# Kernel optimization log

Measured on AMD Instinct MI355X. Metric: run time of the kernel, lower is better.

## Reference

```python
import jax, jax.numpy as jnp
import numpy as np

L, D, H, FF, E, K, S, B = 2, 1024, 16, 4096, 8, 2, 1024, 8
HD = D // H
EPS = 1e-5


def setup_inputs() -> dict:
    key = jax.random.key(0)
    ks = jax.random.split(key, 18)
    sc = 0.02
    inp = {
        "src": jax.random.normal(ks[0], (S, B, D), jnp.float32),
        "pos": jax.random.normal(ks[1], (S, B, D), jnp.float32),
        "qkv_w": jax.random.normal(ks[2], (L, 3 * D, D), jnp.float32) * sc,
        "qkv_b": jnp.zeros((L, 3 * D), jnp.float32),
        "out_w": jax.random.normal(ks[3], (L, D, D), jnp.float32) * sc,
        "out_b": jnp.zeros((L, D), jnp.float32),
        "ln1_w": jnp.ones((L, D), jnp.float32),
        "ln1_b": jnp.zeros((L, D), jnp.float32),
        "ln2_w": jnp.ones((L, D), jnp.float32),
        "ln2_b": jnp.zeros((L, D), jnp.float32),
        "gate_w": jax.random.normal(ks[4], (L, E, D), jnp.float32) * sc,
        "gate_b": jnp.zeros((L, E), jnp.float32),
        "w1": jax.random.normal(ks[5], (L, E, FF, D), jnp.float32) * sc,
        "b1": jnp.zeros((L, E, FF), jnp.float32),
        "w2": jax.random.normal(ks[6], (L, E, D, FF), jnp.float32) * sc,
        "b2": jnp.zeros((L, E, D), jnp.float32),
    }
    return inp


def _ln(x, w, b):
    m = x.mean(-1, keepdims=True)
    v = ((x - m) ** 2).mean(-1, keepdims=True)
    return (x - m) * jax.lax.rsqrt(v + EPS) * w + b


def _attn(src, pos, qkv_w, qkv_b, out_w, out_b):
    qk_in = src + pos  # q = k = with_pos_embed(src, pos); v = src
    wq, wk, wv = qkv_w[:D], qkv_w[D:2 * D], qkv_w[2 * D:]
    bq, bk, bv = qkv_b[:D], qkv_b[D:2 * D], qkv_b[2 * D:]
    q = (qk_in @ wq.T + bq).reshape(S, B, H, HD)
    k = (qk_in @ wk.T + bk).reshape(S, B, H, HD)
    v = (src @ wv.T + bv).reshape(S, B, H, HD)
    scores = jnp.einsum("sbhd,tbhd->bhst", q, k) / jnp.sqrt(jnp.float32(HD))
    a = jax.nn.softmax(scores, axis=-1)
    o = jnp.einsum("bhst,tbhd->sbhd", a, v).reshape(S, B, D)
    return o @ out_w.T + out_b


def _moe(x, gate_w, gate_b, w1, b1, w2, b2):
    T = S * B
    xf = x.reshape(T, D)
    scores = xf @ gate_w.T + gate_b                      # [T, E]
    topv, topi = jax.lax.top_k(scores, K)                # [T, K]
    probs = jax.nn.softmax(topv, axis=-1)                # [T, K]
    # combine weight per (token, expert); experts not in top-k get 0
    cw = jnp.zeros((T, E), xf.dtype).at[jnp.arange(T)[:, None], topi].add(probs)
    out = jnp.zeros_like(xf)
    for e in range(E):  # small fixed loop over experts (structurally distinct GEMMs)
        h = jax.nn.relu(xf @ w1[e].T + b1[e])
        y = h @ w2[e].T + b2[e]
        out = out + cw[:, e:e + 1] * y
    return out.reshape(S, B, D), probs, topi


def _aux(probs, topi):
    usage = jnp.zeros(E, probs.dtype).at[topi.reshape(-1)].add(probs.reshape(-1))
    p = usage / usage.sum()
    return -(p * jnp.log(p + 1e-9)).sum()


def reference(src, pos, qkv_w, qkv_b, out_w, out_b, ln1_w, ln1_b, ln2_w, ln2_b,
              gate_w, gate_b, w1, b1, w2, b2):
    x = src
    aux = jnp.float32(0.0)
    for l in range(L):
        a = _attn(x, pos, qkv_w[l], qkv_b[l], out_w[l], out_b[l])
        x = _ln(x + a, ln1_w[l], ln1_b[l])
        m, probs, topi = _moe(x, gate_w[l], gate_b[l], w1[l], b1[l], w2[l], b2[l])
        aux = aux + (1.0 / L) * _aux(probs, topi)
        x = _ln(x + m, ln2_w[l], ln2_b[l])
    return x, aux
```

## Files before the change

### kernel.cpp

```cpp
#include <hip/hip_runtime.h>

#define L_ 2
#define D_ 1024
#define H_ 16
#define FF_ 4096
#define E_ 8
#define S_ 1024
#define B_ 8
#define T_ (S_*B_)
#define TP_ 17408
#define NBLK_MAX 136
#define HALF_BLK 68

typedef _Float16 half8 __attribute__((ext_vector_type(8)));
typedef _Float16 half4_t __attribute__((ext_vector_type(4)));
typedef float f32x4 __attribute__((ext_vector_type(4)));

__device__ __forceinline__ f32x4 mfma16(half8 a, half8 b, f32x4 c) {
  return __builtin_amdgcn_mfma_f32_16x16x32_f16(a, b, c, 0, 0, 0);
}

struct hl2 { _Float16 h, l; };
__device__ __forceinline__ hl2 split2(float v) {
  hl2 r;
  r.h = (_Float16)v;
  r.l = (_Float16)(v - (float)r.h);
  return r;
}

__device__ __forceinline__ void gll16(const _Float16* g, _Float16* l) {
  __builtin_amdgcn_global_load_lds(
      (const __attribute__((address_space(1))) unsigned int*)g,
      (__attribute__((address_space(3))) unsigned int*)l, 16, 0, 0);
}

template<int NPROD, bool GATHER, bool MOE, bool RELU, int OUT>
__global__ __launch_bounds__(256, 4)
void gemm_pl(const _Float16* __restrict__ Ah, const _Float16* __restrict__ Al,
             const float* __restrict__ B, const float* __restrict__ bias,
             float* __restrict__ C, _Float16* __restrict__ Ch,
             _Float16* __restrict__ Cl,
             int K, int N, long bExpStride, int biasExpStride,
             const int* __restrict__ gtok,
             const int* __restrict__ nblk,
             const unsigned char* __restrict__ blk_e, int mb0)
{
  const int mb = blockIdx.x, nb = blockIdx.y;
  const float* Bp = B;
  const float* biasp = bias;
  if constexpr (MOE) {
    if (mb0 + mb >= *nblk) return;
    const int e = blk_e[mb0 + mb];
    Bp += (long)e * bExpStride;
    biasp += (long)e * biasExpStride;
  }
  const int bcol = nb * 128;
  constexpr int PL = (NPROD == 3) ? 2 : 1;
  __shared__ __align__(16) _Float16 lds[128*32*2*PL];
  _Float16* Ah_s = lds;
  _Float16* Al_s = lds + 128*32;
  _Float16* Bh_s = lds + 128*32*PL;
  _Float16* Bl_s = lds + 128*32*PL + 128*32;

  const int tid = threadIdx.x;
  const int lane = tid & 63, wid = tid >> 6;
  const int wr = wid >> 1, wc = wid & 1;
  const int fr = lane & 15, fkc = lane >> 4;

  f32x4 acc[4][4];
#pragma unroll
  for (int m = 0; m < 4; ++m)
#pragma unroll
    for (int n = 0; n < 4; ++n) acc[m][n] = (f32x4){0.f, 0.f, 0.f, 0.f};

  for (int k0 = 0; k0 < K; k0 += 32) {
    __syncthreads();
#pragma unroll
    for (int ch = wid; ch < 8*PL; ch += 4) {
      const int pl = ch >> 3, rb = (ch & 7) << 4;
      const int rl = rb + (lane >> 2);
      long ar;
      if constexpr (GATHER) ar = gtok[(mb0 + mb)*128 + rl];
      else ar = mb*128 + rl;
      const _Float16* src = (pl ? Al : Ah) + ar*(long)K + k0 + (((lane&3) ^ (rl&3)) << 3);
      _Float16* dst = (pl ? Al_s : Ah_s) + rb*32;
      gll16(src, dst);
    }
#pragma unroll
    for (int i = 0; i < 4; ++i) {
      const int c = i*256 + tid;
      const int row = c >> 3, col = (c & 7) * 4;
      const float4 vb = *(const float4*)&Bp[(long)(bcol + row)*K + k0 + col];
      half4_t hb, lb;
      { hl2 s = split2(vb.x); hb[0] = s.h; lb[0] = s.l; }
      { hl2 s = split2(vb.y); hb[1] = s.h; lb[1] = s.l; }
      { hl2 s = split2(vb.z); hb[2] = s.h; lb[2] = s.l; }
      { hl2 s = split2(vb.w); hb[3] = s.h; lb[3] = s.l; }
      const int sw = (((col >> 3) ^ (row & 3)) << 3) + (col & 4);
      *(half4_t*)&Bh_s[row*32 + sw] = hb;
      if constexpr (NPROD == 3) *(half4_t*)&Bl_s[row*32 + sw] = lb;
    }
    __syncthreads();
    half8 ahf[4], bhf[4], alf[4], blf[4];
#pragma unroll
    for (int m = 0; m < 4; ++m) {
      const int ra = wr*64 + m*16 + fr;
      const int ca = (fkc ^ (ra & 3)) << 3;
      ahf[m] = *(const half8*)&Ah_s[ra*32 + ca];
      if constexpr (NPROD == 3) alf[m] = *(const half8*)&Al_s[ra*32 + ca];
      const int rb2 = wc*64 + m*16 + fr;
      const int cb2 = (fkc ^ (rb2 & 3)) << 3;
      bhf[m] = *(const half8*)&Bh_s[rb2*32 + cb2];
      if constexpr (NPROD == 3) blf[m] = *(const half8*)&Bl_s[rb2*32 + cb2];
    }
#pragma unroll
    for (int m = 0; m < 4; ++m)
#pragma unroll
      for (int n = 0; n < 4; ++n) {
        if constexpr (NPROD == 3) {
          acc[m][n] = mfma16(alf[m], bhf[n], acc[m][n]);
          acc[m][n] = mfma16(ahf[m], blf[n], acc[m][n]);
        }
        acc[m][n] = mfma16(ahf[m], bhf[n], acc[m][n]);
      }
  }
  int cbase;
  if constexpr (MOE) cbase = (OUT != 0) ? mb*128 : (mb0 + mb)*128;
  else cbase = mb*128;
  const int r0 = fkc * 4;
#pragma unroll
  for (int m = 0; m < 4; ++m) {
    const int grow = cbase + wr*64 + m*16 + r0;
#pragma unroll
    for (int n = 0; n < 4; ++n) {
      const int gcol = bcol + wc*64 + n*16 + fr;
      const float bv = biasp[gcol];
#pragma unroll
      for (int r = 0; r < 4; ++r) {
        float v = acc[m][n][r] + bv;
        if constexpr (RELU) v = fmaxf(v, 0.f);
        const long idx = (long)(grow + r) * N + gcol;
        if constexpr (OUT == 0) {
          C[idx] = v;
        } else {
          hl2 s = split2(v);
          Ch[idx] = s.h;
          if constexpr (OUT == 1) Cl[idx] = s.l;
        }
      }
    }
  }
}

__global__ __launch_bounds__(256) void addpos_kernel(const float* __restrict__ x,
    const float* __restrict__ p,
    _Float16* __restrict__ XPh, _Float16* __restrict__ XPl,
    _Float16* __restrict__ XFh, _Float16* __restrict__ XFl)
{
  const long i = (long)blockIdx.x * 256 + threadIdx.x;
  const float4 a = ((const float4*)x)[i];
  const float4 b = ((const float4*)p)[i];
  half4_t fh, fl, ph, pl;
  { hl2 s = split2(a.x); fh[0]=s.h; fl[0]=s.l; }
  { hl2 s = split2(a.y); fh[1]=s.h; fl[1]=s.l; }
  { hl2 s = split2(a.z); fh[2]=s.h; fl[2]=s.l; }
  { hl2 s = split2(a.w); fh[3]=s.h; fl[3]=s.l; }
  { hl2 s = split2(a.x+b.x); ph[0]=s.h; pl[0]=s.l; }
  { hl2 s = split2(a.y+b.y); ph[1]=s.h; pl[1]=s.l; }
  { hl2 s = split2(a.z+b.z); ph[2]=s.h; pl[2]=s.l; }
  { hl2 s = split2(a.w+b.w); ph[3]=s.h; pl[3]=s.l; }
  *(half4_t*)&XFh[i*4] = fh; *(half4_t*)&XFl[i*4] = fl;
  *(half4_t*)&XPh[i*4] = ph; *(half4_t*)&XPl[i*4] = pl;
}

__global__ __launch_bounds__(256) void vtrans_kernel(
    const _Float16* __restrict__ Vh, const _Float16* __restrict__ Vl,
    _Float16* __restrict__ Vth, _Float16* __restrict__ Vtl)
{
  const int st = blockIdx.x, bh = blockIdx.y;
  const int b = bh >> 4, h = bh & 15;
  __shared__ __align__(16) _Float16 th[64*64];
  __shared__ __align__(16) _Float16 tl[64*64];
  const int tid = threadIdx.x;
#pragma unroll
  for (int i = 0; i < 2; ++i) {
    const int r = i*32 + (tid >> 3);
    const int c = tid & 7;
    const long t = (long)(st*64 + r)*8 + b;
    const long ga = t*1024 + h*64 + c*8;
    const int la = r*64 + ((c ^ (r & 7)) << 3);
    *(half8*)&th[la] = *(const half8*)&Vh[ga];
    *(half8*)&tl[la] = *(const half8*)&Vl[ga];
  }
  __syncthreads();
#pragma unroll
  for (int i = 0; i < 2; ++i) {
    const int d = i*32 + (tid >> 3);
    const int sc = tid & 7;
    half8 oh, ol;
#pragma unroll
    for (int j = 0; j < 8; ++j) {
      const int s = sc*8 + j;
      const int la = s*64 + (((d >> 3) ^ (s & 7)) << 3) + (d & 7);
      oh[j] = th[la]; ol[j] = tl[la];
    }
    const long oa = ((long)bh*64 + d)*1024 + st*64 + sc*8;
    *(half8*)&Vth[oa] = oh;
    *(half8*)&Vtl[oa] = ol;
  }
}

__global__ __launch_bounds__(256, 4) void attn_kernel(
    const _Float16* __restrict__ QKh, const _Float16* __restrict__ QKl,
    const _Float16* __restrict__ Vth, const _Float16* __restrict__ Vtl,
    _Float16* __restrict__ Oh, _Float16* __restrict__ Ol)
{
  const int qb = blockIdx.x;
  const int bh = blockIdx.y;
  const int b = bh >> 4, h = bh & 15;
  const int tid = threadIdx.x, lane = tid & 63, wid = tid >> 6;
  const int fr = lane & 15, fkc = lane >> 4;
  __shared__ __align__(16) _Float16 Kh_s[32*64];
  __shared__ __align__(16) _Float16 Kl_s[32*64];
  __shared__ __align__(16) _Float16 Ph[4][16*32];
  __shared__ __align__(16) _Float16 Pl[4][16*32];

  half8 qfh[2], qfl[2];
  {
    const long qbase = ((long)(qb*64 + wid*16 + fr)*8 + b)*2048 + h*64;
#pragma unroll
    for (int dc = 0; dc < 2; ++dc) {
      qfh[dc] = *(const half8*)&QKh[qbase + dc*32 + fkc*8];
      qfl[dc] = *(const half8*)&QKl[qbase + dc*32 + fkc*8];
    }
  }
  f32x4 oacc[4];
#pragma unroll
  for (int c = 0; c < 4; ++c) oacc[c] = (f32x4){0.f,0.f,0.f,0.f};
  float lsum[4] = {0.f,0.f,0.f,0.f};

  for (int kt = 0; kt < 32; ++kt) {
    __syncthreads();
#pragma unroll
    for (int ch = wid; ch < 8; ch += 4) {
      const int pl = ch >> 2, qt = ch & 3;
      const int r = qt*8 + (lane >> 3), c = lane & 7;
      const long t = (long)(kt*32 + r)*8 + b;
      const _Float16* srcp = (pl ? QKl : QKh) + t*2048 + 1024 + h*64 + ((c ^ (r & 7)) << 3);
      _Float16* dstp = (pl ? Kl_s : Kh_s) + (qt << 9);
      gll16(srcp, dstp);
    }
    __syncthreads();

    f32x4 st[2];
    st[0] = (f32x4){0.f,0.f,0.f,0.f}; st[1] = (f32x4){0.f,0.f,0.f,0.f};
#pragma unroll
    for (int tc = 0; tc < 2; ++tc)
#pragma unroll
      for (int dc = 0; dc < 2; ++dc) {
        const int kr = tc*16 + fr;
        const int cc = ((dc*4 + fkc) ^ (kr & 7)) << 3;
        const half8 kfh = *(const half8*)&Kh_s[kr*64 + cc];
        const half8 kfl = *(const half8*)&Kl_s[kr*64 + cc];
        st[tc] = mfma16(qfl[dc], kfh, st[tc]);
        st[tc] = mfma16(qfh[dc], kfl, st[tc]);
        st[tc] = mfma16(qfh[dc], kfh, st[tc]);
      }

    float p0[4], p1[4];
#pragma unroll
    for (int r = 0; r < 4; ++r) {
      p0[r] = __expf(st[0][r] * 0.125f);
      p1[r] = __expf(st[1][r] * 0.125f);
      lsum[r] += p0[r] + p1[r];
    }

#pragma unroll
    for (int r = 0; r < 4; ++r) {
      const int prow = fkc*4 + r;
      hl2 s0 = split2(p0[r]);
      hl2 s1 = split2(p1[r]);
      const int i0 = prow*32 + (((fr>>3) ^ (prow&3)) << 3) + (fr & 7);
      const int c1 = fr + 16;
      const int i1 = prow*32 + (((c1>>3) ^ (prow&3)) << 3) + (c1 & 7);
      Ph[wid][i0] = s0.h;  Pl[wid][i0] = s0.l;
      Ph[wid][i1] = s1.h;  Pl[wid][i1] = s1.l;
    }
    const int ip = fr*32 + ((fkc ^ (fr&3)) << 3);
    const half8 pfh = *(const half8*)&Ph[wid][ip];
    const half8 pfl = *(const half8*)&Pl[wid][ip];

    const long vtb = ((long)bh*64)*1024 + kt*32 + fkc*8;
#pragma unroll
    for (int c = 0; c < 4; ++c) {
      const long va = vtb + (long)(c*16 + fr)*1024;
      const half8 vfh = *(const half8*)&Vth[va];
      const half8 vfl = *(const half8*)&Vtl[va];
      oacc[c] = mfma16(pfl, vfh, oacc[c]);
      oacc[c] = mfma16(pfh, vfl, oacc[c]);
      oacc[c] = mfma16(pfh, vfh, oacc[c]);
    }
  }
#pragma unroll
  for (int r = 0; r < 4; ++r) {
    float l = lsum[r];
    l += __shfl_xor(l, 1); l += __shfl_xor(l, 2);
    l += __shfl_xor(l, 4); l += __shfl_xor(l, 8);
    lsum[r] = l;
  }
#pragma unroll
  for (int c = 0; c < 4; ++c)
#pragma unroll
    for (int r = 0; r < 4; ++r) {
      const int srow = qb*64 + wid*16 + fkc*4 + r;
      const long idx = ((long)srow * B_ + b) * 1024 + h*64 + c*16 + fr;
      hl2 s = split2(oacc[c][r] / lsum[r]);
      Oh[idx] = s.h; Ol[idx] = s.l;
    }
}

template<bool PLANES>
__global__ __launch_bounds__(256) void ln_kernel(
    const float* __restrict__ a, const float* __restrict__ b,
    const float* __restrict__ w, const float* __restrict__ bias,
    float* __restrict__ out, _Float16* __restrict__ Lh, _Float16* __restrict__ Ll)
{
  const int row = blockIdx.x, tid = threadIdx.x;
  const long base = (long)row * D_;
  const float4 va = *(const float4*)&a[base + tid*4];
  const float4 vb = *(const float4*)&b[base + tid*4];
  const float x0 = va.x+vb.x, x1 = va.y+vb.y, x2 = va.z+vb.z, x3 = va.w+vb.w;
  float s = (x0+x1)+(x2+x3);
  float q = (x0*x0+x1*x1)+(x2*x2+x3*x3);
  for (int m = 1; m < 64; m <<= 1) { s += __shfl_xor(s, m); q += __shfl_xor(q, m); }
  __shared__ float rs[4], rq[4];
  const int wid = tid >> 6;
  if ((tid & 63) == 0) { rs[wid] = s; rq[wid] = q; }
  __syncthreads();
  s = (rs[0]+rs[1])+(rs[2]+rs[3]);
  q = (rq[0]+rq[1])+(rq[2]+rq[3]);
  const float mean = s * (1.f/D_);
  const float var = q * (1.f/D_) - mean*mean;
  const float inv = rsqrtf(var + 1e-5f);
  const float4 vw = *(const float4*)&w[tid*4];
  const float4 vbi = *(const float4*)&bias[tid*4];
  float4 r;
  r.x = (x0-mean)*inv*vw.x + vbi.x;
  r.y = (x1-mean)*inv*vw.y + vbi.y;
  r.z = (x2-mean)*inv*vw.z + vbi.z;
  r.w = (x3-mean)*inv*vw.w + vbi.w;
  *(float4*)&out[base + tid*4] = r;
  if constexpr (PLANES) {
    half4_t hh, ll;
    { hl2 t = split2(r.x); hh[0]=t.h; ll[0]=t.l; }
    { hl2 t = split2(r.y); hh[1]=t.h; ll[1]=t.l; }
    { hl2 t = split2(r.z); hh[2]=t.h; ll[2]=t.l; }
    { hl2 t = split2(r.w); hh[3]=t.h; ll[3]=t.l; }
    *(half4_t*)&Lh[base + tid*4] = hh;
    *(half4_t*)&Ll[base + tid*4] = ll;
  }
}

__global__ __launch_bounds__(256) void gate_kernel(const float* __restrict__ x,
    const float* __restrict__ gw, const float* __restrict__ gb, float* __restrict__ sc)
{
  const int t = blockIdx.x * 32 + (threadIdx.x >> 3);
  const int e = threadIdx.x & 7;
  const float* xr = x + (long)t * D_;
  const float* wr = gw + (long)e * D_;
  float a0 = 0, a1 = 0, a2 = 0, a3 = 0;
  for (int d = 0; d < D_; d += 4) {
    const float4 av = *(const float4*)&xr[d];
    const float4 wv = *(const float4*)&wr[d];
    a0 += av.x*wv.x; a1 += av.y*wv.y; a2 += av.z*wv.z; a3 += av.w*wv.w;
  }
  sc[t*E_ + e] = (a0+a1)+(a2+a3) + gb[e];
}

__global__ __launch_bounds__(256) void topk_kernel(const float* __restrict__ sc,
    int* __restrict__ topi, float* __restrict__ tkwt, int* __restrict__ cnt)
{
  const int t = blockIdx.x * 256 + threadIdx.x;
  const float* r = sc + (long)t * E_;
  float v1 = -1e30f, v2 = -1e30f; int i1 = 0, i2 = 0;
#pragma unroll
  for (int e = 0; e < E_; ++e) {
    const float v = r[e];
    if (v > v1) { v2 = v1; i2 = i1; v1 = v; i1 = e; }
    else if (v > v2) { v2 = v; i2 = e; }
  }
  const float e2 = expf(v2 - v1);
  const float inv = 1.f / (1.f + e2);
  topi[t*2] = i1; topi[t*2+1] = i2;
  tkwt[t*2] = inv; tkwt[t*2+1] = e2 * inv;
  atomicAdd(&cnt[i1], 1); atomicAdd(&cnt[i2], 1);
}

__global__ void plan_kernel(const int* __restrict__ cnt, int* __restrict__ cursor,
    int* __restrict__ nblk, unsigned char* __restrict__ blk_e, int* __restrict__ pairs_tok)
{
  __shared__ int soff[9];
  __shared__ int scnt[8];
  if (threadIdx.x == 0) {
    int o = 0;
#pragma unroll
    for (int e = 0; e < E_; ++e) {
      soff[e] = o; cursor[e] = o; scnt[e] = cnt[e];
      o += (cnt[e] + 127) & ~127;
    }
    soff[8] = o;
    *nblk = o >> 7;
  }
  __syncthreads();
  const int total = soff[8];
  for (int bidx = threadIdx.x; bidx < (total >> 7); bidx += 256) {
    const int rb = bidx << 7;
    int e = 0;
    while (e < 7 && rb >= soff[e+1]) ++e;
    blk_e[bidx] = (unsigned char)e;
  }
#pragma unroll
  for (int e = 0; e < E_; ++e) {
    const int s0 = soff[e] + scnt[e], s1 = soff[e+1];
    for (int i = s0 + (int)threadIdx.x; i < s1; i += 256) pairs_tok[i] = 0;
  }
}

__global__ __launch_bounds__(256) void fill_kernel(const int* __restrict__ topi,
    int* __restrict__ cursor, int* __restrict__ pairs_tok, int* __restrict__ tkpos)
{
  const int t = blockIdx.x * 256 + threadIdx.x;
#pragma unroll
  for (int k = 0; k < 2; ++k) {
    const int e = topi[t*2+k];
    const int pos = atomicAdd(&cursor[e], 1);
    pairs_tok[pos] = t;
    tkpos[t*2+k] = pos;
  }
}

__global__ __launch_bounds__(256) void combine_kernel(const float* __restrict__ y,
    const int* __restrict__ tkpos, const float* __restrict__ tkwt, float* __restrict__ out)
{
  const int t = blockIdx.x, d = threadIdx.x * 4;
  const long p0 = tkpos[t*2], p1 = tkpos[t*2+1];
  const float w0 = tkwt[t*2], w1 = tkwt[t*2+1];
  const float4 a = *(const float4*)&y[p0*D_ + d];
  const float4 b = *(const float4*)&y[p1*D_ + d];
  float4 r;
  r.x = w0*a.x + w1*b.x; r.y = w0*a.y + w1*b.y;
  r.z = w0*a.z + w1*b.z; r.w = w0*a.w + w1*b.w;
  *(float4*)&out[(long)t*D_ + d] = r;
}

__global__ void aux_kernel(const int* __restrict__ topi, const float* __restrict__ tkwt,
    float* __restrict__ aux_out, int first)
{
  float u[8] = {0,0,0,0,0,0,0,0};
  for (int i = threadIdx.x; i < T_*2; i += 256) {
    const int e = topi[i]; const float wv = tkwt[i];
#pragma unroll
    for (int k = 0; k < 8; ++k) u[k] += (e == k) ? wv : 0.f;
  }
  __shared__ float red[256];
  float usage[8];
#pragma unroll
  for (int e = 0; e < 8; ++e) {
    red[threadIdx.x] = u[e];
    __syncthreads();
    for (int s = 128; s > 0; s >>= 1) {
      if ((int)threadIdx.x < s) red[threadIdx.x] += red[threadIdx.x + s];
      __syncthreads();
    }
    usage[e] = red[0];
    __syncthreads();
  }
  if (threadIdx.x == 0) {
    float sum = 0;
#pragma unroll
    for (int e = 0; e < 8; ++e) sum += usage[e];
    float Hh = 0;
#pragma unroll
    for (int e = 0; e < 8; ++e) {
      const float p = usage[e] / sum;
      Hh -= p * logf(p + 1e-9f);
    }
    if (first) *aux_out = 0.5f * Hh;
    else *aux_out += 0.5f * Hh;
  }
}

extern "C" void kernel_launch(void* const* d_in, const int* in_sizes, int n_in,
                              void* d_out, int out_size, void* d_ws, size_t ws_size,
                              hipStream_t stream) {
  const float* src    = (const float*)d_in[0];
  const float* pos    = (const float*)d_in[1];
  const float* qkv_w  = (const float*)d_in[2];
  const float* qkv_b  = (const float*)d_in[3];
  const float* out_w  = (const float*)d_in[4];
  const float* out_b  = (const float*)d_in[5];
  const float* ln1_w  = (const float*)d_in[6];
  const float* ln1_b  = (const float*)d_in[7];
  const float* ln2_w  = (const float*)d_in[8];
  const float* ln2_b  = (const float*)d_in[9];
  const float* gate_w = (const float*)d_in[10];
  const float* gate_b = (const float*)d_in[11];
  const float* w1     = (const float*)d_in[12];
  const float* b1     = (const float*)d_in[13];
  const float* w2     = (const float*)d_in[14];
  const float* b2     = (const float*)d_in[15];
  float* out = (float*)d_out;

  char* ws = (char*)d_ws;
  size_t off = 0;
  auto alloc = [&](size_t bytes) -> char* {
    char* p = ws + off;
    off = (off + bytes + 255) & ~(size_t)255;
    return p;
  };
  const size_t TD = (size_t)T_ * D_;
  float* x_master = (float*)alloc(TD*4);
  float* ln1_f    = (float*)alloc(TD*4);
  float* moe_out  = (float*)alloc(TD*4);
  _Float16* L1h   = (_Float16*)alloc(TD*2);
  _Float16* L1l   = (_Float16*)alloc(TD*2);
  float* scores   = (float*)alloc((size_t)T_*E_*4);
  int*   topi     = (int*)alloc((size_t)T_*2*4);
  float* tkwt     = (float*)alloc((size_t)T_*2*4);
  int*   tkpos    = (int*)alloc((size_t)T_*2*4);
  int*   pairs_tok= (int*)alloc((size_t)TP_*4);
  int*   cnt      = (int*)alloc(E_*4);
  int*   cursor   = (int*)alloc(E_*4);
  int*   nblk     = (int*)alloc(256);
  unsigned char* blk_e = (unsigned char*)alloc(256);
  const size_t attn_sz = TD*24;
  const size_t hrows = (size_t)HALF_BLK * 128;
  const size_t moe_sz = hrows*FF_*2*2 + (size_t)TP_*D_*4;
  char* uni = alloc(attn_sz > moe_sz ? attn_sz : moe_sz);
  _Float16* QKh = (_Float16*)uni;
  _Float16* QKl = (_Float16*)(uni + TD*4);
  _Float16* Vh  = (_Float16*)(uni + TD*8);
  _Float16* Vl  = (_Float16*)(uni + TD*10);
  _Float16* Vth = (_Float16*)(uni + TD*12);
  _Float16* Vtl = (_Float16*)(uni + TD*14);
  _Float16* XPh = (_Float16*)(uni + TD*16);
  _Float16* XPl = (_Float16*)(uni + TD*18);
  _Float16* XFh = (_Float16*)(uni + TD*20);
  _Float16* XFl = (_Float16*)(uni + TD*22);
  _Float16* Oh  = XFh;
  _Float16* Ol  = XFl;
  _Float16* Hh  = (_Float16*)uni;
  _Float16* Hl  = (_Float16*)(uni + hrows*FF_*2);
  float* y_buf  = (float*)(uni + hrows*FF_*4);

  for (int l = 0; l < L_; ++l) {
    const float* x_f  = (l == 0) ? src : x_master;
    const float* qkvw = qkv_w + (size_t)l*3*D_*D_;
    const float* qkvb = qkv_b + (size_t)l*3*D_;
    const float* outw = out_w + (size_t)l*D_*D_;
    const float* outb = out_b + (size_t)l*D_;
    const float* w1l  = w1 + (size_t)l*E_*FF_*D_;
    const float* b1l  = b1 + (size_t)l*E_*FF_;
    const float* w2l  = w2 + (size_t)l*E_*D_*FF_;
    const float* b2l  = b2 + (size_t)l*E_*D_;

    addpos_kernel<<<TD/1024, 256, 0, stream>>>(x_f, pos, XPh, XPl, XFh, XFl);
    gemm_pl<3,false,false,false,1><<<dim3(T_/128, 16), 256, 0, stream>>>(
        XPh, XPl, qkvw, qkvb, nullptr, QKh, QKl,
        D_, 2*D_, 0, 0, nullptr, nullptr, nullptr, 0);
    gemm_pl<3,false,false,false,1><<<dim3(T_/128, 8), 256, 0, stream>>>(
        XFh, XFl, qkvw + (size_t)2*D_*D_, qkvb + 2*D_, nullptr, Vh, Vl,
        D_, D_, 0, 0, nullptr, nullptr, nullptr, 0);
    vtrans_kernel<<<dim3(16, 128), 256, 0, stream>>>(Vh, Vl, Vth, Vtl);
    attn_kernel<<<dim3(16, 128), 256, 0, stream>>>(QKh, QKl, Vth, Vtl, Oh, Ol);
    gemm_pl<3,false,false,false,0><<<dim3(T_/128, 8), 256, 0, stream>>>(
        Oh, Ol, outw, outb, moe_out, nullptr, nullptr,
        D_, D_, 0, 0, nullptr, nullptr, nullptr, 0);
    ln_kernel<true><<<T_, 256, 0, stream>>>(x_f, moe_out, ln1_w + (size_t)l*D_,
        ln1_b + (size_t)l*D_, ln1_f, L1h, L1l);
    gate_kernel<<<T_/32, 256, 0, stream>>>(ln1_f, gate_w + (size_t)l*E_*D_,
        gate_b + (size_t)l*E_, scores);
    (void)hipMemsetAsync(cnt, 0, E_*4, stream);
    topk_kernel<<<T_/256, 256, 0, stream>>>(scores, topi, tkwt, cnt);
    plan_kernel<<<1, 256, 0, stream>>>(cnt, cursor, nblk, blk_e, pairs_tok);
    fill_kernel<<<T_/256, 256, 0, stream>>>(topi, cursor, pairs_tok, tkpos);
    for (int half = 0; half < 2; ++half) {
      const int mb0 = half * HALF_BLK;
      if (l == 0) {
        gemm_pl<3,true,true,true,1><<<dim3(HALF_BLK, FF_/128), 256, 0, stream>>>(
            L1h, L1l, w1l, b1l, nullptr, Hh, Hl,
            D_, FF_, (long)FF_*D_, FF_, pairs_tok, nblk, blk_e, mb0);
        gemm_pl<3,false,true,false,0><<<dim3(HALF_BLK, D_/128), 256, 0, stream>>>(
            Hh, Hl, w2l, b2l, y_buf, nullptr, nullptr,
            FF_, D_, (long)D_*FF_, D_, nullptr, nblk, blk_e, mb0);
      } else {
        gemm_pl<1,true,true,true,2><<<dim3(HALF_BLK, FF_/128), 256, 0, stream>>>(
            L1h, L1l, w1l, b1l, nullptr, Hh, nullptr,
            D_, FF_, (long)FF_*D_, FF_, pairs_tok, nblk, blk_e, mb0);
        gemm_pl<1,false,true,false,0><<<dim3(HALF_BLK, D_/128), 256, 0, stream>>>(
            Hh, nullptr, w2l, b2l, y_buf, nullptr, nullptr,
            FF_, D_, (long)D_*FF_, D_, nullptr, nblk, blk_e, mb0);
      }
    }
    combine_kernel<<<T_, 256, 0, stream>>>(y_buf, tkpos, tkwt, moe_out);
    aux_kernel<<<1, 256, 0, stream>>>(topi, tkwt, out + TD, l == 0 ? 1 : 0);
    float* ln2_dst = (l == L_-1) ? out : x_master;
    ln_kernel<false><<<T_, 256, 0, stream>>>(ln1_f, moe_out, ln2_w + (size_t)l*D_,
        ln2_b + (size_t)l*D_, ln2_dst, nullptr, nullptr);
  }
}
```

Measured before the change: 3.727 ms.

## Double-buffer GEMM LDS tiles and prefetch next K-slice during MFMA compute

Restructures the split-fp16 GEMM main loop into a double-buffered pipeline: the next A tile is issued via global_load_lds and the next B tile is loaded into registers before the current MFMAs, then split and written to the other LDS buffer afterward, leaving one barrier per iteration. The LDS layout changes to an MFMA-fragment-linear order so each lane reads a contiguous half8, and per-thread source addresses are precomputed. This aims to hide global memory latency behind compute, at the cost of doubled LDS and more registers, so launch bounds drop from 4 to 2 blocks per SIMD.

```diff
diff --git a/kernel.cpp b/kernel.cpp
--- a/kernel.cpp
+++ b/kernel.cpp
@@ -35,7 +35,7 @@
 }
 
 template<int NPROD, bool GATHER, bool MOE, bool RELU, int OUT>
-__global__ __launch_bounds__(256, 4)
+__global__ __launch_bounds__(256, 2)
 void gemm_pl(const _Float16* __restrict__ Ah, const _Float16* __restrict__ Al,
              const float* __restrict__ B, const float* __restrict__ bias,
              float* __restrict__ C, _Float16* __restrict__ Ch,
@@ -56,16 +56,68 @@
   }
   const int bcol = nb * 128;
   constexpr int PL = (NPROD == 3) ? 2 : 1;
-  __shared__ __align__(16) _Float16 lds[128*32*2*PL];
-  _Float16* Ah_s = lds;
-  _Float16* Al_s = lds + 128*32;
-  _Float16* Bh_s = lds + 128*32*PL;
-  _Float16* Bl_s = lds + 128*32*PL + 128*32;
+  constexpr int BUFH = PL * 8192;
+  constexpr int NCH = PL * 2;
+  __shared__ __align__(16) _Float16 lds[2*BUFH];
 
   const int tid = threadIdx.x;
   const int lane = tid & 63, wid = tid >> 6;
   const int wr = wid >> 1, wc = wid & 1;
-  const int fr = lane & 15, fkc = lane >> 4;
+  const int fkc = lane >> 4;
+
+  const _Float16* asrc[NCH];
+  int adst[NCH];
+#pragma unroll
+  for (int i = 0; i < NCH; ++i) {
+    const int ch = wid + i*4;
+    const int pl = ch >> 3, blk = ch & 7;
+    const int rowin = blk*16 + (lane & 15);
+    long ar;
+    if constexpr (GATHER) ar = gtok[(mb0 + mb)*128 + rowin];
+    else ar = (long)mb*128 + rowin;
+    asrc[i] = (pl ? Al : Ah) + ar*(long)K + ((lane >> 4) << 3);
+    adst[i] = pl*4096 + blk*512;
+  }
+  const float* bsrc[2];
+  int bdst[2];
+#pragma unroll
+  for (int j = 0; j < 2; ++j) {
+    const int s = tid + j*256;
+    const int l = s & 63;
+    const int rowcol = (s >> 6)*16 + (l & 15);
+    const int kh = (l >> 4) << 3;
+    bsrc[j] = Bp + (long)(bcol + rowcol)*K + kh;
+    bdst[j] = PL*4096 + s*8;
+  }
+
+  float4 brg[2][2];
+  auto stageA = [&](int buf, int k0) {
+#pragma unroll
+    for (int i = 0; i < NCH; ++i) gll16(asrc[i] + k0, lds + buf + adst[i]);
+  };
+  auto loadB = [&](int k0) {
+#pragma unroll
+    for (int j = 0; j < 2; ++j) {
+      brg[j][0] = *(const float4*)(bsrc[j] + k0);
+      brg[j][1] = *(const float4*)(bsrc[j] + k0 + 4);
+    }
+  };
+  auto writeB = [&](int buf) {
+#pragma unroll
+    for (int j = 0; j < 2; ++j) {
+      half8 hh; half8 ll;
+      { hl2 s = split2(brg[j][0].x); hh[0]=s.h; ll[0]=s.l; }
+      { hl2 s = split2(brg[j][0].y); hh[1]=s.h; ll[1]=s.l; }
+      { hl2 s = split2(brg[j][0].z); hh[2]=s.h; ll[2]=s.l; }
+      { hl2 s = split2(brg[j][0].w); hh[3]=s.h; ll[3]=s.l; }
+      { hl2 s = split2(brg[j][1].x); hh[4]=s.h; ll[4]=s.l; }
+      { hl2 s = split2(brg[j][1].y); hh[5]=s.h; ll[5]=s.l; }
+      { hl2 s = split2(brg[j][1].z); hh[6]=s.h; ll[6]=s.l; }
+      { hl2 s = split2(brg[j][1].w); hh[7]=s.h; ll[7]=s.l; }
+      *(half8*)&lds[buf + bdst[j]] = hh;
+      if constexpr (NPROD == 3) *(half8*)&lds[buf + bdst[j] + 4096] = ll;
+    }
+  };
 
   f32x4 acc[4][4];
 #pragma unroll
@@ -73,45 +125,23 @@
 #pragma unroll
     for (int n = 0; n < 4; ++n) acc[m][n] = (f32x4){0.f, 0.f, 0.f, 0.f};
 
-  for (int k0 = 0; k0 < K; k0 += 32) {
-    __syncthreads();
-#pragma unroll
-    for (int ch = wid; ch < 8*PL; ch += 4) {
-      const int pl = ch >> 3, rb = (ch & 7) << 4;
-      const int rl = rb + (lane >> 2);
-      long ar;
-      if constexpr (GATHER) ar = gtok[(mb0 + mb)*128 + rl];
-      else ar = mb*128 + rl;
-      const _Float16* src = (pl ? Al : Ah) + ar*(long)K + k0 + (((lane&3) ^ (rl&3)) << 3);
-      _Float16* dst = (pl ? Al_s : Ah_s) + rb*32;
-      gll16(src, dst);
-    }
-#pragma unroll
-    for (int i = 0; i < 4; ++i) {
-      const int c = i*256 + tid;
-      const int row = c >> 3, col = (c & 7) * 4;
-      const float4 vb = *(const float4*)&Bp[(long)(bcol + row)*K + k0 + col];
-      half4_t hb, lb;
-      { hl2 s = split2(vb.x); hb[0] = s.h; lb[0] = s.l; }
-      { hl2 s = split2(vb.y); hb[1] = s.h; lb[1] = s.l; }
-      { hl2 s = split2(vb.z); hb[2] = s.h; lb[2] = s.l; }
-      { hl2 s = split2(vb.w); hb[3] = s.h; lb[3] = s.l; }
-      const int sw = (((col >> 3) ^ (row & 3)) << 3) + (col & 4);
-      *(half4_t*)&Bh_s[row*32 + sw] = hb;
-      if constexpr (NPROD == 3) *(half4_t*)&Bl_s[row*32 + sw] = lb;
-    }
-    __syncthreads();
+  const int NT = K / 32;
+  stageA(0, 0);
+  loadB(0);
+  writeB(0);
+  __syncthreads();
+
+  for (int t = 0; t < NT; ++t) {
+    const int cur = (t & 1) * BUFH;
+    const int nxt = ((t + 1) & 1) * BUFH;
+    if (t + 1 < NT) { stageA(nxt, (t+1)*32); loadB((t+1)*32); }
     half8 ahf[4], bhf[4], alf[4], blf[4];
 #pragma unroll
     for (int m = 0; m < 4; ++m) {
-      const int ra = wr*64 + m*16 + fr;
-      const int ca = (fkc ^ (ra & 3)) << 3;
-      ahf[m] = *(const half8*)&Ah_s[ra*32 + ca];
-      if constexpr (NPROD == 3) alf[m] = *(const half8*)&Al_s[ra*32 + ca];
-      const int rb2 = wc*64 + m*16 + fr;
-      const int cb2 = (fkc ^ (rb2 & 3)) << 3;
-      bhf[m] = *(const half8*)&Bh_s[rb2*32 + cb2];
-      if constexpr (NPROD == 3) blf[m] = *(const half8*)&Bl_s[rb2*32 + cb2];
+      ahf[m] = *(const half8*)&lds[cur + (wr*4 + m)*512 + lane*8];
+      if constexpr (NPROD == 3) alf[m] = *(const half8*)&lds[cur + 4096 + (wr*4 + m)*512 + lane*8];
+      bhf[m] = *(const half8*)&lds[cur + PL*4096 + (wc*4 + m)*512 + lane*8];
+      if constexpr (NPROD == 3) blf[m] = *(const half8*)&lds[cur + PL*4096 + 4096 + (wc*4 + m)*512 + lane*8];
     }
 #pragma unroll
     for (int m = 0; m < 4; ++m)
@@ -123,10 +153,14 @@
         }
         acc[m][n] = mfma16(ahf[m], bhf[n], acc[m][n]);
       }
-  }
+    if (t + 1 < NT) writeB(nxt);
+    __syncthreads();
+  }
+
   int cbase;
   if constexpr (MOE) cbase = (OUT != 0) ? mb*128 : (mb0 + mb)*128;
   else cbase = mb*128;
+  const int fr = lane & 15;
   const int r0 = fkc * 4;
 #pragma unroll
   for (int m = 0; m < 4; ++m) {
```

New measurement: 4.026 ms. 1.08x slower.

## Pre-split fp32 weights into fp16 hi/lo planes and load both operands via LDS DMA

Applied to the files above, without the earlier changes.

Adds a weight-split kernel that converts the QKV, output-projection and expert weights into fp16 hi/lo planes once per layer. The GEMMs then no longer re-read fp32 weights and split them inside every tile. Both A and B tiles are loaded with global_load_lds into a fragment-native LDS layout, using precomputed per-thread source pointers, so the swizzled LDS address math goes away. The cost is extra conversion kernels and roughly 256MB of extra workspace written each layer, plus a lower occupancy hint for the 3-product variant.

```diff
diff --git a/kernel.cpp b/kernel.cpp
--- a/kernel.cpp
+++ b/kernel.cpp
@@ -35,37 +35,58 @@
 }
 
 template<int NPROD, bool GATHER, bool MOE, bool RELU, int OUT>
-__global__ __launch_bounds__(256, 4)
-void gemm_pl(const _Float16* __restrict__ Ah, const _Float16* __restrict__ Al,
-             const float* __restrict__ B, const float* __restrict__ bias,
+__global__ __launch_bounds__(256, NPROD == 3 ? 3 : 4)
+void gemm_qq(const _Float16* __restrict__ Ah, const _Float16* __restrict__ Al,
+             const _Float16* __restrict__ Bh, const _Float16* __restrict__ Bl,
+             const float* __restrict__ bias,
              float* __restrict__ C, _Float16* __restrict__ Ch,
              _Float16* __restrict__ Cl,
-             int K, int N, long bExpStride, int biasExpStride,
+             int K, int N, long bExpStrideH, int biasExpStride,
              const int* __restrict__ gtok,
              const int* __restrict__ nblk,
              const unsigned char* __restrict__ blk_e, int mb0)
 {
   const int mb = blockIdx.x, nb = blockIdx.y;
-  const float* Bp = B;
+  const _Float16* Bhp = Bh;
+  const _Float16* Blp = Bl;
   const float* biasp = bias;
   if constexpr (MOE) {
     if (mb0 + mb >= *nblk) return;
     const int e = blk_e[mb0 + mb];
-    Bp += (long)e * bExpStride;
+    Bhp += (long)e * bExpStrideH;
+    if constexpr (NPROD == 3) Blp += (long)e * bExpStrideH;
     biasp += (long)e * biasExpStride;
   }
   const int bcol = nb * 128;
   constexpr int PL = (NPROD == 3) ? 2 : 1;
-  __shared__ __align__(16) _Float16 lds[128*32*2*PL];
-  _Float16* Ah_s = lds;
-  _Float16* Al_s = lds + 128*32;
-  _Float16* Bh_s = lds + 128*32*PL;
-  _Float16* Bl_s = lds + 128*32*PL + 128*32;
+  __shared__ __align__(16) _Float16 lds[PL*8192];
 
   const int tid = threadIdx.x;
   const int lane = tid & 63, wid = tid >> 6;
   const int wr = wid >> 1, wc = wid & 1;
-  const int fr = lane & 15, fkc = lane >> 4;
+
+  constexpr int PERW = PL * 4;
+  const _Float16* src[PERW];
+  unsigned dstoff[PERW];
+#pragma unroll
+  for (int i = 0; i < PERW; ++i) {
+    const int ch = wid * PERW + i;
+    const bool isB = ch >= PL*8;
+    const int c2 = isB ? ch - PL*8 : ch;
+    const int plane = c2 >> 3, blk = c2 & 7;
+    const int rc = blk*16 + (lane & 15);
+    const int kh = (lane >> 4) * 8;
+    if (!isB) {
+      long r;
+      if constexpr (GATHER) r = gtok[(mb0 + mb)*128 + rc];
+      else r = (long)mb*128 + rc;
+      src[i] = (plane ? Al : Ah) + r*(long)K + kh;
+      dstoff[i] = plane*4096 + blk*512;
+    } else {
+      src[i] = (plane ? Blp : Bhp) + (long)(bcol + rc)*K + kh;
+      dstoff[i] = PL*4096 + plane*4096 + blk*512;
+    }
+  }
 
   f32x4 acc[4][4];
 #pragma unroll
@@ -76,42 +97,17 @@
   for (int k0 = 0; k0 < K; k0 += 32) {
     __syncthreads();
 #pragma unroll
-    for (int ch = wid; ch < 8*PL; ch += 4) {
-      const int pl = ch >> 3, rb = (ch & 7) << 4;
-      const int rl = rb + (lane >> 2);
-      long ar;
-      if constexpr (GATHER) ar = gtok[(mb0 + mb)*128 + rl];
-      else ar = mb*128 + rl;
-      const _Float16* src = (pl ? Al : Ah) + ar*(long)K + k0 + (((lane&3) ^ (rl&3)) << 3);
-      _Float16* dst = (pl ? Al_s : Ah_s) + rb*32;
-      gll16(src, dst);
-    }
-#pragma unroll
-    for (int i = 0; i < 4; ++i) {
-      const int c = i*256 + tid;
-      const int row = c >> 3, col = (c & 7) * 4;
-      const float4 vb = *(const float4*)&Bp[(long)(bcol + row)*K + k0 + col];
-      half4_t hb, lb;
-      { hl2 s = split2(vb.x); hb[0] = s.h; lb[0] = s.l; }
-      { hl2 s = split2(vb.y); hb[1] = s.h; lb[1] = s.l; }
-      { hl2 s = split2(vb.z); hb[2] = s.h; lb[2] = s.l; }
-      { hl2 s = split2(vb.w); hb[3] = s.h; lb[3] = s.l; }
-      const int sw = (((col >> 3) ^ (row & 3)) << 3) + (col & 4);
-      *(half4_t*)&Bh_s[row*32 + sw] = hb;
-      if constexpr (NPROD == 3) *(half4_t*)&Bl_s[row*32 + sw] = lb;
-    }
+    for (int i = 0; i < PERW; ++i) gll16(src[i] + k0, lds + dstoff[i]);
     __syncthreads();
     half8 ahf[4], bhf[4], alf[4], blf[4];
 #pragma unroll
     for (int m = 0; m < 4; ++m) {
-      const int ra = wr*64 + m*16 + fr;
-      const int ca = (fkc ^ (ra & 3)) << 3;
-      ahf[m] = *(const half8*)&Ah_s[ra*32 + ca];
-      if constexpr (NPROD == 3) alf[m] = *(const half8*)&Al_s[ra*32 + ca];
-      const int rb2 = wc*64 + m*16 + fr;
-      const int cb2 = (fkc ^ (rb2 & 3)) << 3;
-      bhf[m] = *(const half8*)&Bh_s[rb2*32 + cb2];
-      if constexpr (NPROD == 3) blf[m] = *(const half8*)&Bl_s[rb2*32 + cb2];
+      ahf[m] = *(const half8*)&lds[(wr*4 + m)*512 + lane*8];
+      bhf[m] = *(const half8*)&lds[PL*4096 + (wc*4 + m)*512 + lane*8];
+      if constexpr (NPROD == 3) {
+        alf[m] = *(const half8*)&lds[4096 + (wr*4 + m)*512 + lane*8];
+        blf[m] = *(const half8*)&lds[PL*4096 + 4096 + (wc*4 + m)*512 + lane*8];
+      }
     }
 #pragma unroll
     for (int m = 0; m < 4; ++m)
@@ -124,10 +120,12 @@
         acc[m][n] = mfma16(ahf[m], bhf[n], acc[m][n]);
       }
   }
+
   int cbase;
   if constexpr (MOE) cbase = (OUT != 0) ? mb*128 : (mb0 + mb)*128;
   else cbase = mb*128;
-  const int r0 = fkc * 4;
+  const int fr = lane & 15;
+  const int r0 = (lane >> 4) * 4;
 #pragma unroll
   for (int m = 0; m < 4; ++m) {
     const int grow = cbase + wr*64 + m*16 + r0;
@@ -150,6 +148,21 @@
       }
     }
   }
+}
+
+template<bool WL>
+__global__ __launch_bounds__(256) void wsplit_kernel(const float* __restrict__ w,
+    _Float16* __restrict__ wh, _Float16* __restrict__ wl)
+{
+  const long i = ((long)blockIdx.x * 256 + threadIdx.x) * 4;
+  const float4 v = *(const float4*)&w[i];
+  half4_t h, l;
+  { hl2 s = split2(v.x); h[0]=s.h; l[0]=s.l; }
+  { hl2 s = split2(v.y); h[1]=s.h; l[1]=s.l; }
+  { hl2 s = split2(v.z); h[2]=s.h; l[2]=s.l; }
+  { hl2 s = split2(v.w); h[3]=s.h; l[3]=s.l; }
+  *(half4_t*)&wh[i] = h;
+  if constexpr (WL) *(half4_t*)&wl[i] = l;
 }
 
 __global__ __launch_bounds__(256) void addpos_kernel(const float* __restrict__ x,
@@ -524,6 +537,11 @@
   float* moe_out  = (float*)alloc(TD*4);
   _Float16* L1h   = (_Float16*)alloc(TD*2);
   _Float16* L1l   = (_Float16*)alloc(TD*2);
+  const size_t QW = (size_t)3*D_*D_;
+  _Float16* DQh = (_Float16*)alloc(QW*2);
+  _Float16* DQl = (_Float16*)alloc(QW*2);
+  _Float16* DOh = (_Float16*)alloc((size_t)D_*D_*2);
+  _Float16* DOl = (_Float16*)alloc((size_t)D_*D_*2);
   float* scores   = (float*)alloc((size_t)T_*E_*4);
   int*   topi     = (int*)alloc((size_t)T_*2*4);
   float* tkwt     = (float*)alloc((size_t)T_*2*4);
@@ -535,7 +553,8 @@
   unsigned char* blk_e = (unsigned char*)alloc(256);
   const size_t attn_sz = TD*24;
   const size_t hrows = (size_t)HALF_BLK * 128;
-  const size_t moe_sz = hrows*FF_*2*2 + (size_t)TP_*D_*4;
+  const size_t WE = (size_t)E_*FF_*D_;
+  const size_t moe_sz = hrows*FF_*2*2 + (size_t)TP_*D_*4 + WE*2*4;
   char* uni = alloc(attn_sz > moe_sz ? attn_sz : moe_sz);
   _Float16* QKh = (_Float16*)uni;
   _Float16* QKl = (_Float16*)(uni + TD*4);
@@ -552,6 +571,10 @@
   _Float16* Hh  = (_Float16*)uni;
   _Float16* Hl  = (_Float16*)(uni + hrows*FF_*2);
   float* y_buf  = (float*)(uni + hrows*FF_*4);
+  _Float16* W1h = (_Float16*)(uni + hrows*FF_*4 + (size_t)TP_*D_*4);
+  _Float16* W1l = W1h + WE;
+  _Float16* W2h = W1l + WE;
+  _Float16* W2l = W2h + WE;
 
   for (int l = 0; l < L_; ++l) {
     const float* x_f  = (l == 0) ? src : x_master;
@@ -559,23 +582,32 @@
     const float* qkvb = qkv_b + (size_t)l*3*D_;
     const float* outw = out_w + (size_t)l*D_*D_;
     const float* outb = out_b + (size_t)l*D_;
-    const float* w1l  = w1 + (size_t)l*E_*FF_*D_;
+    const float* w1l  = w1 + (size_t)l*WE;
     const float* b1l  = b1 + (size_t)l*E_*FF_;
-    const float* w2l  = w2 + (size_t)l*E_*D_*FF_;
+    const float* w2l  = w2 + (size_t)l*WE;
     const float* b2l  = b2 + (size_t)l*E_*D_;
 
+    wsplit_kernel<true><<<QW/1024, 256, 0, stream>>>(qkvw, DQh, DQl);
+    wsplit_kernel<true><<<D_*D_/1024, 256, 0, stream>>>(outw, DOh, DOl);
     addpos_kernel<<<TD/1024, 256, 0, stream>>>(x_f, pos, XPh, XPl, XFh, XFl);
-    gemm_pl<3,false,false,false,1><<<dim3(T_/128, 16), 256, 0, stream>>>(
-        XPh, XPl, qkvw, qkvb, nullptr, QKh, QKl,
+    gemm_qq<3,false,false,false,1><<<dim3(T_/128, 16), 256, 0, stream>>>(
+        XPh, XPl, DQh, DQl, qkvb, nullptr, QKh, QKl,
         D_, 2*D_, 0, 0, nullptr, nullptr, nullptr, 0);
-    gemm_pl<3,false,false,false,1><<<dim3(T_/128, 8), 256, 0, stream>>>(
-        XFh, XFl, qkvw + (size_t)2*D_*D_, qkvb + 2*D_, nullptr, Vh, Vl,
-        D_, D_, 0, 0, nullptr, nullptr, nullptr, 0);
+    gemm_qq<3,false,false,false,1><<<dim3(T_/128, 8), 256, 0, stream>>>(
+        XFh, XFl, DQh + (size_t)2*D_*D_, DQl + (size_t)2*D_*D_, qkvb + 2*D_,
+        nullptr, Vh, Vl, D_, D_, 0, 0, nullptr, nullptr, nullptr, 0);
     vtrans_kernel<<<dim3(16, 128), 256, 0, stream>>>(Vh, Vl, Vth, Vtl);
     attn_kernel<<<dim3(16, 128), 256, 0, stream>>>(QKh, QKl, Vth, Vtl, Oh, Ol);
-    gemm_pl<3,false,false,false,0><<<dim3(T_/128, 8), 256, 0, stream>>>(
-        Oh, Ol, outw, outb, moe_out, nullptr, nullptr,
+    gemm_qq<3,false,false,false,0><<<dim3(T_/128, 8), 256, 0, stream>>>(
+        Oh, Ol, DOh, DOl, outb, moe_out, nullptr, nullptr,
         D_, D_, 0, 0, nullptr, nullptr, nullptr, 0);
+    if (l == 0) {
+      wsplit_kernel<true><<<WE/1024, 256, 0, stream>>>(w1l, W1h, W1l);
+      wsplit_kernel<true><<<WE/1024, 256, 0, stream>>>(w2l, W2h, W2l);
+    } else {
+      wsplit_kernel<false><<<WE/1024, 256, 0, stream>>>(w1l, W1h, nullptr);
+      wsplit_kernel<false><<<WE/1024, 256, 0, stream>>>(w2l, W2h, nullptr);
+    }
     ln_kernel<true><<<T_, 256, 0, stream>>>(x_f, moe_out, ln1_w + (size_t)l*D_,
         ln1_b + (size_t)l*D_, ln1_f, L1h, L1l);
     gate_kernel<<<T_/32, 256, 0, stream>>>(ln1_f, gate_w + (size_t)l*E_*D_,
@@ -587,18 +619,18 @@
     for (int half = 0; half < 2; ++half) {
       const int mb0 = half * HALF_BLK;
       if (l == 0) {
-        gemm_pl<3,true,true,true,1><<<dim3(HALF_BLK, FF_/128), 256, 0, stream>>>(
-            L1h, L1l, w1l, b1l, nullptr, Hh, Hl,
+        gemm_qq<3,true,true,true,1><<<dim3(HALF_BLK, FF_/128), 256, 0, stream>>>(
+            L1h, L1l, W1h, W1l, b1l, nullptr, Hh, Hl,
             D_, FF_, (long)FF_*D_, FF_, pairs_tok, nblk, blk_e, mb0);
-        gemm_pl<3,false,true,false,0><<<dim3(HALF_BLK, D_/128), 256, 0, stream>>>(
-            Hh, Hl, w2l, b2l, y_buf, nullptr, nullptr,
+        gemm_qq<3,false,true,false,0><<<dim3(HALF_BLK, D_/128), 256, 0, stream>>>(
+            Hh, Hl, W2h, W2l, b2l, y_buf, nullptr, nullptr,
             FF_, D_, (long)D_*FF_, D_, nullptr, nblk, blk_e, mb0);
       } else {
-        gemm_pl<1,true,true,true,2><<<dim3(HALF_BLK, FF_/128), 256, 0, stream>>>(
-            L1h, L1l, w1l, b1l, nullptr, Hh, nullptr,
+        gemm_qq<1,true,true,true,2><<<dim3(HALF_BLK, FF_/128), 256, 0, stream>>>(
+            L1h, nullptr, W1h, nullptr, b1l, nullptr, Hh, nullptr,
             D_, FF_, (long)FF_*D_, FF_, pairs_tok, nblk, blk_e, mb0);
-        gemm_pl<1,false,true,false,0><<<dim3(HALF_BLK, D_/128), 256, 0, stream>>>(
-            Hh, nullptr, w2l, b2l, y_buf, nullptr, nullptr,
+        gemm_qq<1,false,true,false,0><<<dim3(HALF_BLK, D_/128), 256, 0, stream>>>(
+            Hh, nullptr, W2h, nullptr, b2l, y_buf, nullptr, nullptr,
             FF_, D_, (long)D_*FF_, D_, nullptr, nblk, blk_e, mb0);
       }
     }
```

Result: slower. 4.110 ms (+10.3%).
